# Performance work log

Measured on AMD Instinct MI355X. Metric: run time of the kernel, lower is better.

Reference implementation:

```python
import jax, jax.numpy as jnp
import numpy as np

ARITY = 4
DEPTH = 8  # leaves live at level DEPTH; levels 0..DEPTH, BFS layout
N_NODES = (ARITY ** (DEPTH + 1) - 1) // (ARITY - 1)  # 87381
V, E, H = 1024, 128, 128


def _offset(level):
    return (ARITY ** level - 1) // (ARITY - 1)


def _lstm_final(seq, w_ih, w_hh, b):
    # seq: [T, B, E_in] -> final hidden state [B, H] (torch LSTM cell, gate order i,f,g,o)
    B = seq.shape[1]
    Hh = w_hh.shape[1]
    xg = jnp.einsum('tbe,ge->tbg', seq, w_ih) + b  # precompute input projections [T,B,4H]

    def step(carry, g_t):
        h, c = carry
        g = g_t + h @ w_hh.T
        i, f, gg, o = jnp.split(g, 4, axis=-1)
        c = jax.nn.sigmoid(f) * c + jax.nn.sigmoid(i) * jnp.tanh(gg)
        h = jax.nn.sigmoid(o) * jnp.tanh(c)
        return (h, c), None

    init = (jnp.zeros((B, Hh), seq.dtype), jnp.zeros((B, Hh), seq.dtype))
    (h, _), _ = jax.lax.scan(step, init, xg)
    return h


def setup_inputs():
    key = jax.random.key(0)
    ks = jax.random.split(key, 12)
    s = 0.1
    labels = jax.random.randint(ks[0], (N_NODES,), 0, V)
    emb = jax.random.normal(ks[1], (V, E), jnp.float32) * s
    emb = emb.at[0].set(0.0)  # padding_idx=0
    mk = lambda k, shp: jax.random.normal(k, shp, jnp.float32) * s
    return {
        'labels': labels, 'emb': emb,
        'w_ih_f': mk(ks[2], (4 * H, E)), 'w_hh_f': mk(ks[3], (4 * H, H)),
        'b_ih_f': mk(ks[4], (4 * H,)), 'b_hh_f': mk(ks[5], (4 * H,)),
        'w_ih_b': mk(ks[6], (4 * H, E)), 'w_hh_b': mk(ks[7], (4 * H, H)),
        'b_ih_b': mk(ks[8], (4 * H,)), 'b_hh_b': mk(ks[9], (4 * H,)),
        'lin_w': mk(ks[10], (E, 2 * H)), 'lin_b': mk(ks[11], (E,)),
    }


def reference(labels, emb, w_ih_f, w_hh_f, b_ih_f, b_hh_f,
              w_ih_b, w_hh_b, b_ih_b, b_hh_b, lin_w, lin_b):
    # padding row is frozen at zero (padding_idx=0 semantics)
    emb = emb.at[0].set(0.0)
    node_emb = emb[labels]  # [N, E]
    bf = b_ih_f + b_hh_f
    bb = b_ih_b + b_hh_b
    enc = jnp.zeros((N_NODES, E), node_emb.dtype)
    # level-by-level dynamic batching: identical math to per-node recursion
    for level in range(DEPTH, -1, -1):
        start = _offset(level)
        count = ARITY ** level
        x = node_emb[start:start + count]  # [C, E]
        if level == DEPTH:
            seq = jnp.stack([x, x])  # leaves: [node, node] -> [2, C, E]
        else:
            cstart = _offset(level + 1)
            ch = enc[cstart:cstart + count * ARITY]
            ch = ch.reshape(count, ARITY, E).transpose(1, 0, 2)  # [K, C, E]
            seq = jnp.concatenate([x[None], ch, x[None]], axis=0)  # [K+2, C, E]
        h_f = _lstm_final(seq, w_ih_f, w_hh_f, bf)          # forward direction
        h_b = _lstm_final(seq[::-1], w_ih_b, w_hh_b, bb)    # reverse direction
        out = jnp.tanh(jnp.concatenate([h_f, h_b], axis=-1) @ lin_w.T + lin_b)
        enc = enc.at[start:start + count].set(out)
    return enc[0]  # root encoding, shape [E]
```

## Files before the change

### kernel.cpp

```cpp
#include <hip/hip_runtime.h>
#include <hip/hip_bf16.h>

typedef __attribute__((ext_vector_type(8))) short bf16x8;
typedef __attribute__((ext_vector_type(4))) float f32x4;

__device__ __forceinline__ ushort f2bf(float f) {
  union { float f; unsigned u; } v; v.f = f;
  unsigned u = v.u;
  return (ushort)((u + 0x7FFFu + ((u >> 16) & 1u)) >> 16);
}
__device__ __forceinline__ float bf2f(ushort u) {
  union { unsigned u; float f; } v; v.u = ((unsigned)u) << 16;
  return v.f;
}
__device__ __forceinline__ float fsig(float x) {
  return __builtin_amdgcn_rcpf(1.0f + __expf(-x));
}
__device__ __forceinline__ float ftnh(float x) {
  float e = __expf(2.0f * x);
  return 1.0f - 2.0f * __builtin_amdgcn_rcpf(e + 1.0f);
}
__device__ __forceinline__ f32x4 MF(bf16x8 a, bf16x8 b, f32x4 c) {
  return __builtin_amdgcn_mfma_f32_16x16x32_bf16(a, b, c, 0, 0, 0);
}

__global__ __launch_bounds__(256) void repack_all2(
    const float* __restrict__ wihf, const float* __restrict__ whhf,
    const float* __restrict__ wihb, const float* __restrict__ whhb,
    const float* __restrict__ emb, const float* __restrict__ linw,
    ushort* __restrict__ wall) {
  int i = blockIdx.x * 256 + threadIdx.x;
  if (i < 131072) {
    int e = i & 7, f = (i >> 3) & 15, lane = (i >> 7) & 63, w = (i >> 13) & 7,
        d = (i >> 16) & 1;
    int nt = f >> 2, kk = f & 3;
    int pcol = w * 64 + nt * 16 + (lane & 15);
    int g = (pcol >> 4) & 3, h = (pcol >> 6) * 16 + (pcol & 15);
    int k = kk * 32 + (lane >> 4) * 8 + e;
    const float* src = d ? whhb : whhf;
    wall[i] = f2bf(src[(g * 128 + h) * 128 + k]);
  } else if (i < 262144) {
    int r = i - 131072;
    int e = r & 7, lane = (r >> 3) & 63, kk = (r >> 9) & 3, j = (r >> 11) & 7,
        wq = (r >> 14) & 3, d = (r >> 16) & 1;
    int pcol = wq * 128 + j * 16 + (lane & 15);
    int g = (pcol >> 4) & 3, h = (pcol >> 6) * 16 + (pcol & 15);
    int k = kk * 32 + (lane >> 4) * 8 + e;
    const float* src = d ? wihb : wihf;
    wall[i] = f2bf(src[(g * 128 + h) * 128 + k]);
  } else if (i < 294912) {
    int r = i - 262144;
    int e = r & 7, lane = (r >> 3) & 63, kk = (r >> 9) & 7, w = (r >> 12) & 7;
    int col = w * 16 + (lane & 15);
    int k = kk * 32 + (lane >> 4) * 8 + e;
    wall[i] = f2bf(linw[col * 256 + k]);
  } else if (i < 425984) {
    int r = i - 294912;
    wall[i] = f2bf(emb[r]);
  }
}

__global__ __launch_bounds__(512) void gate_vocab(
    const ushort* __restrict__ emb_bf, const ushort* __restrict__ wihrep,
    ushort* __restrict__ gxv) {
  __shared__ __align__(16) ushort sT[2048];
  const int tid = threadIdx.x;
  const int w = tid >> 6, l = tid & 63, hlo = l & 15, lg = l >> 4;
  const int r0 = lg * 4, k0 = lg * 8;
  const int v0 = blockIdx.x * 16;
  {
    int row = tid >> 5, col0 = (tid & 31) * 4;
    *(ushort4*)(sT + row * 128 + (col0 ^ ((row & 7) << 3))) =
        *(const ushort4*)(emb_bf + (size_t)(v0 + row) * 128 + col0);
  }
  __syncthreads();
  const int d = w >> 2, wq = w & 3;
  const ushort* wp = wihrep + (size_t)(d * 4 + wq) * 16384 + l * 8;
  bf16x8 wf[32];
#pragma unroll
  for (int j = 0; j < 8; ++j)
#pragma unroll
    for (int kk = 0; kk < 4; ++kk)
      wf[j * 4 + kk] = *(const bf16x8*)(wp + j * 2048 + kk * 512);
  bf16x8 a[4];
#pragma unroll
  for (int kk = 0; kk < 4; ++kk)
    a[kk] = *(const bf16x8*)(sT + hlo * 128 + ((kk * 32 + k0) ^ ((hlo & 7) << 3)));
  f32x4 acc[8];
#pragma unroll
  for (int j = 0; j < 8; ++j) { f32x4 z = {0.f, 0.f, 0.f, 0.f}; acc[j] = z; }
#pragma unroll
  for (int kk = 0; kk < 4; ++kk)
#pragma unroll
    for (int j = 0; j < 8; ++j) acc[j] = MF(a[kk], wf[j * 4 + kk], acc[j]);
#pragma unroll
  for (int p = 0; p < 2; ++p)
#pragma unroll
    for (int rg = 0; rg < 4; ++rg) {
      int row = v0 + r0 + rg;
      int hid = (wq * 2 + p) * 16 + hlo;
      ushort4 q = {f2bf(acc[p * 4 + 0][rg]), f2bf(acc[p * 4 + 1][rg]),
                   f2bf(acc[p * 4 + 2][rg]), f2bf(acc[p * 4 + 3][rg])};
      *(ushort4*)(gxv + (size_t)row * 1024 + d * 512 + hid * 4) = q;
    }
}

__global__ __launch_bounds__(512) void leaf_scan(
    const ushort* __restrict__ gxv, const ushort* __restrict__ whhrep,
    const float* __restrict__ bihf, const float* __restrict__ bhhf,
    const float* __restrict__ bihb, const float* __restrict__ bhhb,
    ushort* __restrict__ hL) {
  __shared__ __align__(16) ushort sH[2048];
  const int tid = threadIdx.x;
  const int w = tid >> 6, l = tid & 63, hlo = l & 15, lg = l >> 4;
  const int r0 = lg * 4, k0 = lg * 8;
  const int hcol = w * 16 + hlo;
  const int d = blockIdx.y;
  const int v0 = blockIdx.x * 16;

  bf16x8 whh[16];
  {
    const ushort* p = whhrep + d * 65536 + w * 8192 + l * 128;
#pragma unroll
    for (int f = 0; f < 16; ++f) whh[f] = *(const bf16x8*)(p + f * 8);
  }
  const float* bih = d ? bihb : bihf;
  const float* bhh = d ? bhhb : bhhf;
  float bs[4];
#pragma unroll
  for (int nt = 0; nt < 4; ++nt) bs[nt] = bih[nt * 128 + hcol] + bhh[nt * 128 + hcol];

  ushort4 xg[4];
#pragma unroll
  for (int rg = 0; rg < 4; ++rg)
    xg[rg] = *(const ushort4*)(gxv + (size_t)(v0 + r0 + rg) * 1024 + d * 512 + hcol * 4);

  float c_st[4], hn[4];
#pragma unroll
  for (int rg = 0; rg < 4; ++rg) {
    float g0 = bf2f(((const ushort*)&xg[rg])[0]) + bs[0];
    float g1 = bf2f(((const ushort*)&xg[rg])[1]) + bs[1];
    float g2 = bf2f(((const ushort*)&xg[rg])[2]) + bs[2];
    float g3 = bf2f(((const ushort*)&xg[rg])[3]) + bs[3];
    float c = fsig(g0) * ftnh(g2);
    c_st[rg] = c;
    hn[rg] = fsig(g3) * ftnh(c);
  }
#pragma unroll
  for (int rg = 0; rg < 4; ++rg) {
    int rr = r0 + rg;
    sH[rr * 128 + (hcol ^ ((rr & 7) << 3))] = f2bf(hn[rg]);
  }
  __syncthreads();
  f32x4 a4[4];
#pragma unroll
  for (int rg = 0; rg < 4; ++rg)
#pragma unroll
    for (int nt = 0; nt < 4; ++nt)
      a4[nt][rg] = bf2f(((const ushort*)&xg[rg])[nt]) + bs[nt];
  bf16x8 ah[4];
#pragma unroll
  for (int kk = 0; kk < 4; ++kk)
    ah[kk] = *(const bf16x8*)(sH + hlo * 128 + ((kk * 32 + k0) ^ ((hlo & 7) << 3)));
#pragma unroll
  for (int kk = 0; kk < 4; ++kk)
#pragma unroll
    for (int nt = 0; nt < 4; ++nt) a4[nt] = MF(ah[kk], whh[nt * 4 + kk], a4[nt]);
#pragma unroll
  for (int rg = 0; rg < 4; ++rg) {
    float iv = fsig(a4[0][rg]);
    float fv = fsig(a4[1][rg]);
    float gv = ftnh(a4[2][rg]);
    float ov = fsig(a4[3][rg]);
    float c = fv * c_st[rg] + iv * gv;
    hn[rg] = ov * ftnh(c);
    hL[((size_t)d * 1024 + (v0 + r0 + rg)) * 128 + hcol] = f2bf(hn[rg]);
  }
}

__global__ __launch_bounds__(512) void leaf_fin(
    const ushort* __restrict__ hL, const ushort* __restrict__ linrep,
    const float* __restrict__ linb, const ushort* __restrict__ wihrep,
    ushort* __restrict__ gcv) {
  __shared__ __align__(16) ushort sT[2048];
  const int tid = threadIdx.x;
  const int w = tid >> 6, l = tid & 63, hlo = l & 15, lg = l >> 4;
  const int r0 = lg * 4, k0 = lg * 8;
  const int v0 = blockIdx.x * 16;
  const float lb = linb[w * 16 + hlo];
  f32x4 hac = {lb, lb, lb, lb};
#pragma unroll
  for (int kk = 0; kk < 8; ++kk) {
    bf16x8 lf = *(const bf16x8*)(linrep + w * 4096 + kk * 512 + l * 8);
    bf16x8 af = *(const bf16x8*)(hL + ((size_t)(kk >> 2) * 1024 + v0 + hlo) * 128 +
                                 (kk & 3) * 32 + k0);
    hac = MF(af, lf, hac);
  }
#pragma unroll
  for (int rg = 0; rg < 4; ++rg) {
    int rr = r0 + rg;
    sT[rr * 128 + ((w * 16 + hlo) ^ ((rr & 7) << 3))] = f2bf(ftnh(hac[rg]));
  }
  __syncthreads();
  const int d = w >> 2, wq = w & 3;
  const ushort* wp = wihrep + (size_t)(d * 4 + wq) * 16384 + l * 8;
  bf16x8 wf[32];
#pragma unroll
  for (int j = 0; j < 8; ++j)
#pragma unroll
    for (int kk = 0; kk < 4; ++kk)
      wf[j * 4 + kk] = *(const bf16x8*)(wp + j * 2048 + kk * 512);
  bf16x8 a[4];
#pragma unroll
  for (int kk = 0; kk < 4; ++kk)
    a[kk] = *(const bf16x8*)(sT + hlo * 128 + ((kk * 32 + k0) ^ ((hlo & 7) << 3)));
  f32x4 acc[8];
#pragma unroll
  for (int j = 0; j < 8; ++j) { f32x4 z = {0.f, 0.f, 0.f, 0.f}; acc[j] = z; }
#pragma unroll
  for (int kk = 0; kk < 4; ++kk)
#pragma unroll
    for (int j = 0; j < 8; ++j) acc[j] = MF(a[kk], wf[j * 4 + kk], acc[j]);
#pragma unroll
  for (int p = 0; p < 2; ++p)
#pragma unroll
    for (int rg = 0; rg < 4; ++rg) {
      int row = v0 + r0 + rg;
      int hid = (wq * 2 + p) * 16 + hlo;
      ushort4 q = {f2bf(acc[p * 4 + 0][rg]), f2bf(acc[p * 4 + 1][rg]),
                   f2bf(acc[p * 4 + 2][rg]), f2bf(acc[p * 4 + 3][rg])};
      *(ushort4*)(gcv + (size_t)row * 1024 + d * 512 + hid * 4) = q;
    }
}

__global__ __launch_bounds__(512) void scan7_k(
    const int* __restrict__ labels, const ushort* __restrict__ gxv,
    const ushort* __restrict__ gcv, const ushort* __restrict__ whhrep,
    const float* __restrict__ bihf, const float* __restrict__ bhhf,
    const float* __restrict__ bihb, const float* __restrict__ bhhb,
    ushort* __restrict__ h7) {
  __shared__ __align__(16) ushort sH[2][2048];
  const int tid = threadIdx.x;
  const int w = tid >> 6, l = tid & 63, hlo = l & 15, lg = l >> 4;
  const int r0 = lg * 4, k0 = lg * 8;
  const int hcol = w * 16 + hlo;
  const int d = blockIdx.y;
  const int g = blockIdx.x;

  bf16x8 whh[16];
  {
    const ushort* p = whhrep + d * 65536 + w * 8192 + l * 128;
#pragma unroll
    for (int f = 0; f < 16; ++f) whh[f] = *(const bf16x8*)(p + f * 8);
  }
  const float* bih = d ? bihb : bihf;
  const float* bhh = d ? bhhb : bhhf;
  float bs[4];
#pragma unroll
  for (int nt = 0; nt < 4; ++nt) bs[nt] = bih[nt * 128 + hcol] + bhh[nt * 128 + hcol];

  int nn[4];
  ushort4 xg[4];
#pragma unroll
  for (int rg = 0; rg < 4; ++rg) {
    nn[rg] = g * 16 + r0 + rg;
    int xr = labels[5461 + nn[rg]];
    xg[rg] = *(const ushort4*)(gxv + (size_t)xr * 1024 + d * 512 + hcol * 4);
  }
  ushort4 cg[2][4];
  {
    const int ci = d ? 3 : 0;
#pragma unroll
    for (int rg = 0; rg < 4; ++rg) {
      int cl = labels[21845 + nn[rg] * 4 + ci];
      cg[1][rg] = *(const ushort4*)(gcv + (size_t)cl * 1024 + d * 512 + hcol * 4);
    }
  }
  float c_st[4], hn[4];
#pragma unroll
  for (int t = 0; t < 6; ++t) {
    const bool isx = (t == 0) || (t == 5);
    f32x4 a4[4];
#pragma unroll
    for (int rg = 0; rg < 4; ++rg) {
      ushort4 u = isx ? xg[rg] : cg[t & 1][rg];
#pragma unroll
      for (int nt = 0; nt < 4; ++nt)
        a4[nt][rg] = bf2f(((const ushort*)&u)[nt]) + bs[nt];
    }
    if (t >= 1 && t <= 3) {
      const int ci = d ? (3 - t) : t;
#pragma unroll
      for (int rg = 0; rg < 4; ++rg) {
        int cl = labels[21845 + nn[rg] * 4 + ci];
        cg[(t + 1) & 1][rg] =
            *(const ushort4*)(gcv + (size_t)cl * 1024 + d * 512 + hcol * 4);
      }
    }
    if (t > 0) {
      bf16x8 ah[4];
#pragma unroll
      for (int kk = 0; kk < 4; ++kk)
        ah[kk] = *(const bf16x8*)(&sH[(t + 1) & 1][0] + hlo * 128 +
                                  ((kk * 32 + k0) ^ ((hlo & 7) << 3)));
#pragma unroll
      for (int kk = 0; kk < 4; ++kk)
#pragma unroll
        for (int nt = 0; nt < 4; ++nt) a4[nt] = MF(ah[kk], whh[nt * 4 + kk], a4[nt]);
    }
#pragma unroll
    for (int rg = 0; rg < 4; ++rg) {
      float iv = fsig(a4[0][rg]);
      float fv = fsig(a4[1][rg]);
      float gv = ftnh(a4[2][rg]);
      float ov = fsig(a4[3][rg]);
      float c = (t == 0) ? (iv * gv) : (fv * c_st[rg] + iv * gv);
      c_st[rg] = c;
      hn[rg] = ov * ftnh(c);
    }
    if (t < 5) {
#pragma unroll
      for (int rg = 0; rg < 4; ++rg) {
        int rr = r0 + rg;
        sH[t & 1][rr * 128 + (hcol ^ ((rr & 7) << 3))] = f2bf(hn[rg]);
      }
      __syncthreads();
    } else {
#pragma unroll
      for (int rg = 0; rg < 4; ++rg)
        h7[((size_t)d * 16384 + nn[rg]) * 128 + hcol] = f2bf(hn[rg]);
    }
  }
}

__device__ __forceinline__ void scan_embed(
    int g, int d, int cnt, const int* __restrict__ xlab,
    const ushort* __restrict__ gxv, const ushort* __restrict__ hsrc,
    const ushort* __restrict__ wihrep, const ushort* __restrict__ whhrep,
    const ushort* __restrict__ linrep, const float* __restrict__ linb,
    const float* __restrict__ bihf, const float* __restrict__ bhhf,
    const float* __restrict__ bihb, const float* __restrict__ bhhb,
    ushort* __restrict__ hdst, ushort* sG, ushort* sHb, ushort* sT) {
  const int tid = threadIdx.x;
  const int w = tid >> 6, l = tid & 63, hlo = l & 15, lg = l >> 4;
  const int r0 = lg * 4, k0 = lg * 8;
  const int hcol = w * 16 + hlo;
  const int ccnt = 4 * cnt;

  bf16x8 wf[16];
  {
    const ushort* wp = wihrep + (size_t)(d * 4 + (w >> 1)) * 16384 +
                       (size_t)((w & 1) * 4) * 2048 + l * 8;
#pragma unroll
    for (int jj = 0; jj < 4; ++jj)
#pragma unroll
      for (int kk = 0; kk < 4; ++kk)
        wf[jj * 4 + kk] = *(const bf16x8*)(wp + jj * 2048 + kk * 512);
  }
  const float lb = linb[hcol];
  const int ntile = min(4, (ccnt - g * 64 + 15) >> 4);
  for (int tt = 0; tt < ntile; ++tt) {
    f32x4 hac = {lb, lb, lb, lb};
    int cr = g * 64 + tt * 16 + hlo;
    if (cr >= ccnt) cr = ccnt - 1;
#pragma unroll
    for (int kk = 0; kk < 8; ++kk) {
      bf16x8 lf = *(const bf16x8*)(linrep + w * 4096 + kk * 512 + l * 8);
      bf16x8 af = *(const bf16x8*)(hsrc + ((size_t)(kk >> 2) * ccnt + cr) * 128 +
                                   (kk & 3) * 32 + k0);
      hac = MF(af, lf, hac);
    }
    __syncthreads();
#pragma unroll
    for (int rg = 0; rg < 4; ++rg) {
      int rr = r0 + rg;
      sT[rr * 128 + (hcol ^ ((rr & 7) << 3))] = f2bf(ftnh(hac[rg]));
    }
    __syncthreads();
    bf16x8 a[4];
#pragma unroll
    for (int kk = 0; kk < 4; ++kk)
      a[kk] = *(const bf16x8*)(sT + hlo * 128 + ((kk * 32 + k0) ^ ((hlo & 7) << 3)));
    f32x4 acc[4];
#pragma unroll
    for (int jj = 0; jj < 4; ++jj) { f32x4 z = {0.f, 0.f, 0.f, 0.f}; acc[jj] = z; }
#pragma unroll
    for (int kk = 0; kk < 4; ++kk)
#pragma unroll
      for (int jj = 0; jj < 4; ++jj) acc[jj] = MF(a[kk], wf[jj * 4 + kk], acc[jj]);
    const int hid = (w >> 1) * 32 + (w & 1) * 16 + hlo;
#pragma unroll
    for (int rg = 0; rg < 4; ++rg) {
      int lrow = tt * 16 + r0 + rg;
      int sw = ((((lrow >> 4) & 3) ^ ((lrow >> 2) & 3)) << 4);
      ushort4 q = {f2bf(acc[0][rg]), f2bf(acc[1][rg]), f2bf(acc[2][rg]),
                   f2bf(acc[3][rg])};
      *(ushort4*)(sG + lrow * 512 + ((hid * 4) ^ sw)) = q;
    }
  }
  __syncthreads();

  bf16x8 whh[16];
  {
    const ushort* p = whhrep + d * 65536 + w * 8192 + l * 128;
#pragma unroll
    for (int f = 0; f < 16; ++f) whh[f] = *(const bf16x8*)(p + f * 8);
  }
  const float* bih = d ? bihb : bihf;
  const float* bhh = d ? bhhb : bhhf;
  float bs[4];
#pragma unroll
  for (int nt = 0; nt < 4; ++nt) bs[nt] = bih[nt * 128 + hcol] + bhh[nt * 128 + hcol];

  int nn[4];
  ushort4 xg[4];
#pragma unroll
  for (int rg = 0; rg < 4; ++rg) {
    nn[rg] = g * 16 + r0 + rg;
    int cl = nn[rg] < cnt ? nn[rg] : cnt - 1;
    int xr = xlab[cl];
    xg[rg] = *(const ushort4*)(gxv + (size_t)xr * 1024 + d * 512 + hcol * 4);
  }
  float c_st[4], hn[4];
#pragma unroll
  for (int t = 0; t < 6; ++t) {
    const bool isx = (t == 0) || (t == 5);
    f32x4 a4[4];
#pragma unroll
    for (int rg = 0; rg < 4; ++rg) {
      ushort4 u;
      if (isx) {
        u = xg[rg];
      } else {
        const int ci = d ? (4 - t) : (t - 1);
        int lrow = (r0 + rg) * 4 + ci;
        int sw = ((((lrow >> 4) & 3) ^ ((lrow >> 2) & 3)) << 4);
        u = *(const ushort4*)(sG + lrow * 512 + ((hcol * 4) ^ sw));
      }
#pragma unroll
      for (int nt = 0; nt < 4; ++nt)
        a4[nt][rg] = bf2f(((const ushort*)&u)[nt]) + bs[nt];
    }
    if (t > 0) {
      bf16x8 ah[4];
#pragma unroll
      for (int kk = 0; kk < 4; ++kk)
        ah[kk] = *(const bf16x8*)(sHb + ((t + 1) & 1) * 2048 + hlo * 128 +
                                  ((kk * 32 + k0) ^ ((hlo & 7) << 3)));
#pragma unroll
      for (int kk = 0; kk < 4; ++kk)
#pragma unroll
        for (int nt = 0; nt < 4; ++nt) a4[nt] = MF(ah[kk], whh[nt * 4 + kk], a4[nt]);
    }
#pragma unroll
    for (int rg = 0; rg < 4; ++rg) {
      float iv = fsig(a4[0][rg]);
      float fv = fsig(a4[1][rg]);
      float gv = ftnh(a4[2][rg]);
      float ov = fsig(a4[3][rg]);
      float c = (t == 0) ? (iv * gv) : (fv * c_st[rg] + iv * gv);
      c_st[rg] = c;
      hn[rg] = ov * ftnh(c);
    }
    if (t < 5) {
#pragma unroll
      for (int rg = 0; rg < 4; ++rg) {
        int rr = r0 + rg;
        sHb[(t & 1) * 2048 + rr * 128 + (hcol ^ ((rr & 7) << 3))] = f2bf(hn[rg]);
      }
      __syncthreads();
    } else {
#pragma unroll
      for (int rg = 0; rg < 4; ++rg)
        if (nn[rg] < cnt)
          hdst[((size_t)d * cnt + nn[rg]) * 128 + hcol] = f2bf(hn[rg]);
    }
  }
}

__global__ __launch_bounds__(512) void scan6_k(
    const int* __restrict__ xlab, const ushort* __restrict__ gxv,
    const ushort* __restrict__ h7, const ushort* __restrict__ wihrep,
    const ushort* __restrict__ whhrep, const ushort* __restrict__ linrep,
    const float* __restrict__ linb, const float* __restrict__ bihf,
    const float* __restrict__ bhhf, const float* __restrict__ bihb,
    const float* __restrict__ bhhb, ushort* __restrict__ h6) {
  __shared__ __align__(16) ushort sG[32768];
  __shared__ __align__(16) ushort sH[2][2048];
  __shared__ __align__(16) ushort sT[2048];
  scan_embed(blockIdx.x, blockIdx.y, 4096, xlab, gxv, h7, wihrep, whhrep,
             linrep, linb, bihf, bhhf, bihb, bhhb, h6, sG, &sH[0][0], sT);
}

__device__ __forceinline__ void gsync(unsigned* cnt, unsigned target) {
  __syncthreads();
  if (threadIdx.x == 0) {
    __builtin_amdgcn_fence(__ATOMIC_RELEASE, "agent");
    __hip_atomic_fetch_add(cnt, 1u, __ATOMIC_RELAXED, __HIP_MEMORY_SCOPE_AGENT);
    while (__hip_atomic_load(cnt, __ATOMIC_RELAXED, __HIP_MEMORY_SCOPE_AGENT) <
           target)
      __builtin_amdgcn_s_sleep(2);
    __builtin_amdgcn_fence(__ATOMIC_ACQUIRE, "agent");
  }
  __syncthreads();
}

__global__ __launch_bounds__(512) void coop_tail(
    const int* __restrict__ labels, const ushort* __restrict__ gxv,
    ushort* __restrict__ hpool, const ushort* __restrict__ wihrep,
    const ushort* __restrict__ whhrep, const ushort* __restrict__ linrep,
    const float* __restrict__ linb, const float* __restrict__ bihf,
    const float* __restrict__ bhhf, const float* __restrict__ bihb,
    const float* __restrict__ bhhb, float* __restrict__ outp,
    unsigned* __restrict__ cnt) {
  __shared__ __align__(16) ushort sG[32768];
  __shared__ __align__(16) ushort sH[2][2048];
  __shared__ __align__(16) ushort sT[2048];
  const int cnts[6] = {1024, 256, 64, 16, 4, 1};
  const int xoffs[6] = {341, 85, 21, 5, 1, 0};
  const unsigned srcoff[6] = {4194304u, 5242880u, 5505024u, 5570560u, 5586944u,
                              5591040u};
  const unsigned dstoff[6] = {5242880u, 5505024u, 5570560u, 5586944u, 5591040u,
                              5592064u};
  for (int p = 0; p < 6; ++p) {
    const int c = cnts[p];
    const int ntasks = 2 * ((c + 15) >> 4);
    for (int task = blockIdx.x; task < ntasks; task += gridDim.x)
      scan_embed(task >> 1, task & 1, c, labels + xoffs[p], gxv,
                 hpool + srcoff[p], wihrep, whhrep, linrep, linb, bihf, bhhf,
                 bihb, bhhb, hpool + dstoff[p], sG, &sH[0][0], sT);
    gsync(cnt, (unsigned)(p + 1) * gridDim.x);
  }
  if (blockIdx.x == 0) {
    const int tid = threadIdx.x;
    const int w = tid >> 6, l = tid & 63, hlo = l & 15, lg = l >> 4;
    const ushort* h0 = hpool + 5592064u;
    const float lb = linb[w * 16 + hlo];
    f32x4 hac = {lb, lb, lb, lb};
#pragma unroll
    for (int kk = 0; kk < 8; ++kk) {
      bf16x8 lf = *(const bf16x8*)(linrep + w * 4096 + kk * 512 + l * 8);
      bf16x8 af =
          *(const bf16x8*)(h0 + (size_t)(kk >> 2) * 128 + (kk & 3) * 32 + lg * 8);
      hac = MF(af, lf, hac);
    }
    if (lg == 0) outp[w * 16 + hlo] = ftnh(hac[0]);
  }
}

extern "C" void kernel_launch(void* const* d_in, const int* in_sizes, int n_in,
                              void* d_out, int out_size, void* d_ws, size_t ws_size,
                              hipStream_t stream) {
  const int* labels = (const int*)d_in[0];
  const float* emb = (const float*)d_in[1];
  const float* w_ih_f = (const float*)d_in[2];
  const float* w_hh_f = (const float*)d_in[3];
  const float* b_ih_f = (const float*)d_in[4];
  const float* b_hh_f = (const float*)d_in[5];
  const float* w_ih_b = (const float*)d_in[6];
  const float* w_hh_b = (const float*)d_in[7];
  const float* b_ih_b = (const float*)d_in[8];
  const float* b_hh_b = (const float*)d_in[9];
  const float* lin_w = (const float*)d_in[10];
  const float* lin_b = (const float*)d_in[11];
  float* out = (float*)d_out;

  unsigned* cnt = (unsigned*)d_ws;
  ushort* W = (ushort*)d_ws;
  ushort* gxv = W + 512;
  ushort* gcv = gxv + 1048576;
  ushort* hpool = gcv + 1048576;
  ushort* hL = hpool + 5592320;
  ushort* wall = hL + 262144;
  ushort* whhrep = wall;
  ushort* wihrep = wall + 131072;
  ushort* linrep = wall + 262144;
  ushort* emb_bf = wall + 294912;
  ushort* h7 = hpool;
  ushort* h6 = hpool + 4194304;

  hipMemsetAsync(cnt, 0, 4, stream);
  repack_all2<<<1664, 256, 0, stream>>>(w_ih_f, w_hh_f, w_ih_b, w_hh_b, emb,
                                        lin_w, wall);
  gate_vocab<<<64, 512, 0, stream>>>(emb_bf, wihrep, gxv);
  leaf_scan<<<dim3(64, 2), 512, 0, stream>>>(gxv, whhrep, b_ih_f, b_hh_f,
                                             b_ih_b, b_hh_b, hL);
  leaf_fin<<<64, 512, 0, stream>>>(hL, linrep, lin_b, wihrep, gcv);
  scan7_k<<<dim3(1024, 2), 512, 0, stream>>>(labels, gxv, gcv, whhrep, b_ih_f,
                                             b_hh_f, b_ih_b, b_hh_b, h7);
  scan6_k<<<dim3(256, 2), 512, 0, stream>>>(labels + 1365, gxv, h7, wihrep,
                                            whhrep, linrep, lin_b, b_ih_f,
                                            b_hh_f, b_ih_b, b_hh_b, h6);
  coop_tail<<<128, 512, 0, stream>>>(labels, gxv, hpool, wihrep, whhrep, linrep,
                                     lin_b, b_ih_f, b_hh_f, b_ih_b, b_hh_b, out,
                                     cnt);
}
```

Before: 294.7 us.

## Fold level-6 scan into persistent tail kernel with sharded grid barrier

Removes the separate scan6 launch and runs level 6 as the first phase of a single persistent kernel with 256 blocks. The single global atomic counter barrier becomes 16 padded counters plus a release flag that block 0 sets, which cuts atomic contention. The last three tiny levels (16, 4 and 1 nodes) now run on block 0 alone, so three grid barriers become block-local fences. The persistent kernel relies on all 256 blocks being co-resident, and the small levels become serial within one block.

```diff
diff --git a/kernel.cpp b/kernel.cpp
--- a/kernel.cpp
+++ b/kernel.cpp
@@ -139,7 +139,6 @@
 #pragma unroll
   for (int rg = 0; rg < 4; ++rg) {
     float g0 = bf2f(((const ushort*)&xg[rg])[0]) + bs[0];
-    float g1 = bf2f(((const ushort*)&xg[rg])[1]) + bs[1];
     float g2 = bf2f(((const ushort*)&xg[rg])[2]) + bs[2];
     float g3 = bf2f(((const ushort*)&xg[rg])[3]) + bs[3];
     float c = fsig(g0) * ftnh(g2);
@@ -478,74 +477,86 @@
   }
 }
 
-__global__ __launch_bounds__(512) void scan6_k(
-    const int* __restrict__ xlab, const ushort* __restrict__ gxv,
-    const ushort* __restrict__ h7, const ushort* __restrict__ wihrep,
-    const ushort* __restrict__ whhrep, const ushort* __restrict__ linrep,
-    const float* __restrict__ linb, const float* __restrict__ bihf,
-    const float* __restrict__ bhhf, const float* __restrict__ bihb,
-    const float* __restrict__ bhhb, ushort* __restrict__ h6) {
-  __shared__ __align__(16) ushort sG[32768];
-  __shared__ __align__(16) ushort sH[2][2048];
-  __shared__ __align__(16) ushort sT[2048];
-  scan_embed(blockIdx.x, blockIdx.y, 4096, xlab, gxv, h7, wihrep, whhrep,
-             linrep, linb, bihf, bhhf, bihb, bhhb, h6, sG, &sH[0][0], sT);
-}
-
-__device__ __forceinline__ void gsync(unsigned* cnt, unsigned target) {
+__device__ __forceinline__ void gbar(unsigned* bar, int epoch, unsigned nblocks) {
   __syncthreads();
   if (threadIdx.x == 0) {
     __builtin_amdgcn_fence(__ATOMIC_RELEASE, "agent");
-    __hip_atomic_fetch_add(cnt, 1u, __ATOMIC_RELAXED, __HIP_MEMORY_SCOPE_AGENT);
-    while (__hip_atomic_load(cnt, __ATOMIC_RELAXED, __HIP_MEMORY_SCOPE_AGENT) <
-           target)
-      __builtin_amdgcn_s_sleep(2);
+    __hip_atomic_fetch_add(&bar[(blockIdx.x & 15) * 32], 1u, __ATOMIC_RELAXED,
+                           __HIP_MEMORY_SCOPE_AGENT);
+    unsigned* flag = &bar[512];
+    if (blockIdx.x == 0) {
+      unsigned sum;
+      do {
+        sum = 0;
+#pragma unroll
+        for (int i = 0; i < 16; ++i)
+          sum += __hip_atomic_load(&bar[i * 32], __ATOMIC_RELAXED,
+                                   __HIP_MEMORY_SCOPE_AGENT);
+      } while (sum < nblocks * (unsigned)epoch);
+      __hip_atomic_store(flag, (unsigned)epoch, __ATOMIC_RELAXED,
+                         __HIP_MEMORY_SCOPE_AGENT);
+    } else {
+      while (__hip_atomic_load(flag, __ATOMIC_RELAXED,
+                               __HIP_MEMORY_SCOPE_AGENT) < (unsigned)epoch)
+        __builtin_amdgcn_s_sleep(1);
+    }
     __builtin_amdgcn_fence(__ATOMIC_ACQUIRE, "agent");
   }
   __syncthreads();
 }
 
-__global__ __launch_bounds__(512) void coop_tail(
+__global__ __launch_bounds__(512) void coop_tail2(
     const int* __restrict__ labels, const ushort* __restrict__ gxv,
     ushort* __restrict__ hpool, const ushort* __restrict__ wihrep,
     const ushort* __restrict__ whhrep, const ushort* __restrict__ linrep,
     const float* __restrict__ linb, const float* __restrict__ bihf,
     const float* __restrict__ bhhf, const float* __restrict__ bihb,
     const float* __restrict__ bhhb, float* __restrict__ outp,
-    unsigned* __restrict__ cnt) {
+    unsigned* __restrict__ bar) {
   __shared__ __align__(16) ushort sG[32768];
   __shared__ __align__(16) ushort sH[2][2048];
   __shared__ __align__(16) ushort sT[2048];
-  const int cnts[6] = {1024, 256, 64, 16, 4, 1};
-  const int xoffs[6] = {341, 85, 21, 5, 1, 0};
-  const unsigned srcoff[6] = {4194304u, 5242880u, 5505024u, 5570560u, 5586944u,
-                              5591040u};
-  const unsigned dstoff[6] = {5242880u, 5505024u, 5570560u, 5586944u, 5591040u,
-                              5592064u};
-  for (int p = 0; p < 6; ++p) {
-    const int c = cnts[p];
-    const int ntasks = 2 * ((c + 15) >> 4);
+  const int pcnt[4] = {4096, 1024, 256, 64};
+  const int pxoff[4] = {1365, 341, 85, 21};
+  const unsigned psrc[4] = {0u, 4194304u, 5242880u, 5505024u};
+  const unsigned pdst[4] = {4194304u, 5242880u, 5505024u, 5570560u};
+  for (int p = 0; p < 4; ++p) {
+    const int c = pcnt[p];
+    const int ntasks = 2 * (c >> 4);
     for (int task = blockIdx.x; task < ntasks; task += gridDim.x)
-      scan_embed(task >> 1, task & 1, c, labels + xoffs[p], gxv,
-                 hpool + srcoff[p], wihrep, whhrep, linrep, linb, bihf, bhhf,
-                 bihb, bhhb, hpool + dstoff[p], sG, &sH[0][0], sT);
-    gsync(cnt, (unsigned)(p + 1) * gridDim.x);
-  }
-  if (blockIdx.x == 0) {
-    const int tid = threadIdx.x;
-    const int w = tid >> 6, l = tid & 63, hlo = l & 15, lg = l >> 4;
-    const ushort* h0 = hpool + 5592064u;
-    const float lb = linb[w * 16 + hlo];
-    f32x4 hac = {lb, lb, lb, lb};
-#pragma unroll
-    for (int kk = 0; kk < 8; ++kk) {
-      bf16x8 lf = *(const bf16x8*)(linrep + w * 4096 + kk * 512 + l * 8);
-      bf16x8 af =
-          *(const bf16x8*)(h0 + (size_t)(kk >> 2) * 128 + (kk & 3) * 32 + lg * 8);
-      hac = MF(af, lf, hac);
-    }
-    if (lg == 0) outp[w * 16 + hlo] = ftnh(hac[0]);
-  }
+      scan_embed(task >> 1, task & 1, c, labels + pxoff[p], gxv,
+                 hpool + psrc[p], wihrep, whhrep, linrep, linb, bihf, bhhf,
+                 bihb, bhhb, hpool + pdst[p], sG, &sH[0][0], sT);
+    gbar(bar, p + 1, gridDim.x);
+  }
+  if (blockIdx.x != 0) return;
+
+  const int scnt[3] = {16, 4, 1};
+  const int sxoff[3] = {5, 1, 0};
+  const unsigned ssrc[3] = {5570560u, 5586944u, 5591040u};
+  const unsigned sdst[3] = {5586944u, 5591040u, 5592064u};
+  for (int p = 0; p < 3; ++p) {
+    for (int d = 0; d < 2; ++d)
+      scan_embed(0, d, scnt[p], labels + sxoff[p], gxv, hpool + ssrc[p],
+                 wihrep, whhrep, linrep, linb, bihf, bhhf, bihb, bhhb,
+                 hpool + sdst[p], sG, &sH[0][0], sT);
+    __syncthreads();
+    __builtin_amdgcn_fence(__ATOMIC_ACQ_REL, "agent");
+    __syncthreads();
+  }
+  const int tid = threadIdx.x;
+  const int w = tid >> 6, l = tid & 63, hlo = l & 15, lg = l >> 4;
+  const ushort* h0 = hpool + 5592064u;
+  const float lb = linb[w * 16 + hlo];
+  f32x4 hac = {lb, lb, lb, lb};
+#pragma unroll
+  for (int kk = 0; kk < 8; ++kk) {
+    bf16x8 lf = *(const bf16x8*)(linrep + w * 4096 + kk * 512 + l * 8);
+    bf16x8 af =
+        *(const bf16x8*)(h0 + (size_t)(kk >> 2) * 128 + (kk & 3) * 32 + lg * 8);
+    hac = MF(af, lf, hac);
+  }
+  if (lg == 0) outp[w * 16 + hlo] = ftnh(hac[0]);
 }
 
 extern "C" void kernel_launch(void* const* d_in, const int* in_sizes, int n_in,
@@ -565,9 +576,9 @@
   const float* lin_b = (const float*)d_in[11];
   float* out = (float*)d_out;
 
-  unsigned* cnt = (unsigned*)d_ws;
+  unsigned* bar = (unsigned*)d_ws;
   ushort* W = (ushort*)d_ws;
-  ushort* gxv = W + 512;
+  ushort* gxv = W + 2048;
   ushort* gcv = gxv + 1048576;
   ushort* hpool = gcv + 1048576;
   ushort* hL = hpool + 5592320;
@@ -577,9 +588,8 @@
   ushort* linrep = wall + 262144;
   ushort* emb_bf = wall + 294912;
   ushort* h7 = hpool;
-  ushort* h6 = hpool + 4194304;
-
-  hipMemsetAsync(cnt, 0, 4, stream);
+
+  hipMemsetAsync(bar, 0, 4096, stream);
   repack_all2<<<1664, 256, 0, stream>>>(w_ih_f, w_hh_f, w_ih_b, w_hh_b, emb,
                                         lin_w, wall);
   gate_vocab<<<64, 512, 0, stream>>>(emb_bf, wihrep, gxv);
@@ -588,10 +598,7 @@
   leaf_fin<<<64, 512, 0, stream>>>(hL, linrep, lin_b, wihrep, gcv);
   scan7_k<<<dim3(1024, 2), 512, 0, stream>>>(labels, gxv, gcv, whhrep, b_ih_f,
                                              b_hh_f, b_ih_b, b_hh_b, h7);
-  scan6_k<<<dim3(256, 2), 512, 0, stream>>>(labels + 1365, gxv, h7, wihrep,
-                                            whhrep, linrep, lin_b, b_ih_f,
-                                            b_hh_f, b_ih_b, b_hh_b, h6);
-  coop_tail<<<128, 512, 0, stream>>>(labels, gxv, hpool, wihrep, whhrep, linrep,
-                                     lin_b, b_ih_f, b_hh_f, b_ih_b, b_hh_b, out,
-                                     cnt);
-}
+  coop_tail2<<<256, 512, 0, stream>>>(labels, gxv, hpool, wihrep, whhrep,
+                                      linrep, lin_b, b_ih_f, b_hh_f, b_ih_b,
+                                      b_hh_b, out, bar);
+}
```

Result: slower. 341.9 us (+16.0%).
